# Optimization experiments

Measured on AMD Instinct MI355X. Metric: run time of the kernel, lower is better.

The kernel has to match this reference:

```python
import jax, jax.numpy as jnp
import numpy as np

B = 262144
HID = 256
HEADS = 8


def setup_inputs() -> dict:
    key = jax.random.key(0)
    ks = jax.random.split(key, 8)
    s = 1.0 / np.sqrt(HID)
    return {
        "fine_messages": jax.random.normal(ks[0], (B, HID), jnp.float32),
        "coarse_messages": jax.random.normal(ks[1], (B, HID), jnp.float32),
        "motif_features": jax.random.normal(ks[2], (B, HID), jnp.float32),
        "Wq": jax.random.normal(ks[3], (HID, HID), jnp.float32) * s,
        "Wk": jax.random.normal(ks[4], (HID, HID), jnp.float32) * s,
        "Wv": jax.random.normal(ks[5], (HID, HID), jnp.float32) * s,
        "Wo": jax.random.normal(ks[6], (HID, HID), jnp.float32) * s,
        "bo": jax.random.normal(ks[7], (HID,), jnp.float32) * s,
        "heads": HEADS,
    }


def reference(fine_messages, coarse_messages, motif_features, Wq, Wk, Wv, Wo, bo, heads):
    b, hid = motif_features.shape
    d_k = hid // heads
    # K/V share the same pre-projection input: [fine; coarse] -> (B, 2, hid)
    kv_in = jnp.stack([fine_messages, coarse_messages], axis=1)
    # torch Linear(x) = x @ W.T (no bias on q/k/v projections)
    q = (motif_features @ Wq.T).reshape(b, heads, d_k)          # (B, H, d_k) single query
    k = (kv_in @ Wk.T).reshape(b, 2, heads, d_k)                # (B, 2, H, d_k)
    v = (kv_in @ Wv.T).reshape(b, 2, heads, d_k)
    # NOTE: original divides by d_k, not sqrt(d_k)
    scores = jnp.einsum("bhd,bshd->bhs", q, k) / d_k            # (B, H, 2)
    att = jax.nn.softmax(scores, axis=-1)
    out = jnp.einsum("bhs,bshd->bhd", att, v).reshape(b, hid)   # (B, hid)
    return out @ Wo.T + bo
```

## Files before the change

### kernel.cpp

```cpp
#include <hip/hip_runtime.h>

#define B_TOT 262144
#define HID   256
#define NHEAD 8
#define BR    64
#define NTHR  256

typedef __bf16 bf16_t;
typedef __attribute__((ext_vector_type(8))) __bf16 bf16x8;
typedef __attribute__((ext_vector_type(4))) __bf16 bf16x4;
typedef __attribute__((ext_vector_type(4))) float  f32x4;

#define QKV_BYTES (384 * 1024)

static __device__ __forceinline__ f32x4 mfma16(bf16x8 a, bf16x8 b, f32x4 c) {
  return __builtin_amdgcn_mfma_f32_16x16x32_bf16(a, b, c, 0, 0, 0);
}

static __device__ __forceinline__ bf16x8 cvt8(float4 a, float4 b) {
  bf16x8 r;
  r[0] = (bf16_t)a.x; r[1] = (bf16_t)a.y; r[2] = (bf16_t)a.z; r[3] = (bf16_t)a.w;
  r[4] = (bf16_t)b.x; r[5] = (bf16_t)b.y; r[6] = (bf16_t)b.z; r[7] = (bf16_t)b.w;
  return r;
}

static __device__ __forceinline__ bf16x8 pin8(bf16x8 v) {
  f32x4 t = __builtin_bit_cast(f32x4, v);
  asm volatile("" : "+v"(t));
  return __builtin_bit_cast(bf16x8, t);
}

typedef __attribute__((address_space(3))) void lds_void;
typedef __attribute__((address_space(1))) void gbl_void;
static __device__ __forceinline__ void gload_lds16(const void* g, void* l) {
  __builtin_amdgcn_global_load_lds((gbl_void*)g, (lds_void*)l, 16, 0, 0);
}

__global__ __launch_bounds__(256) void pack_weights(
    const float* __restrict__ Wq, const float* __restrict__ Wk,
    const float* __restrict__ Wv, const float* __restrict__ Wo,
    bf16_t* __restrict__ ws) {
  const int t     = blockIdx.x * 256 + threadIdx.x;
  const int lane  = t & 63;
  const int chunk = t >> 6;
  const int l15 = lane & 15, lg = lane >> 4;
  const float* src;
  int row, col;
  if (chunk < 384) {
    const int slot = chunk % 6;
    const int hk   = chunk / 6;
    const int wi = slot >> 1, half = slot & 1;
    const int h = hk >> 3, ks = hk & 7;
    src = (wi == 0) ? Wq : (wi == 1) ? Wk : Wv;
    row = h * 32 + (l15 >> 2) * 8 + half * 4 + (l15 & 3);
    col = ks * 32 + lg * 8;
  } else {
    const int c  = chunk - 384;
    const int ks = c >> 4, jt = c & 15;
    src = Wo;
    row = jt * 16 + l15;
    col = ks * 32 + lg * 8;
  }
  const float* p = src + (size_t)row * HID + col;
  const float4 a = *(const float4*)p;
  const float4 b = *(const float4*)(p + 4);
  *(bf16x8*)(ws + (size_t)t * 8) = cvt8(a, b);
}

__global__ __launch_bounds__(NTHR, 2) void fused_local_aug(
    const float* __restrict__ fine, const float* __restrict__ coarse,
    const float* __restrict__ motif, const bf16_t* __restrict__ wpk,
    const float* __restrict__ bo, float* __restrict__ out) {
  __shared__ char wbuf[49152];

  const int tid  = threadIdx.x;
  const int lane = tid & 63;
  const int wave = tid >> 6;
  const int l15  = lane & 15;
  const int lg   = lane >> 4;
  const size_t row0 = (size_t)blockIdx.x * BR;
  const size_t mrow = row0 + wave * 16 + l15;

  auto stage = [&](int ph) {
    if (ph >= 24) return;
    char* dst = wbuf + (ph & 1) * 24576 + tid * 16;
    if (ph < 16) {
      const char* src = (const char*)wpk + (ph >> 1) * 49152 + (ph & 1) * 24576 + tid * 16;
#pragma unroll
      for (int i = 0; i < 6; ++i)
        gload_lds16(src + i * 4096, dst + i * 4096);
    } else {
      const char* src = (const char*)wpk + QKV_BYTES + (ph - 16) * 16384 + tid * 16;
#pragma unroll
      for (int i = 0; i < 4; ++i)
        gload_lds16(src + i * 4096, dst + i * 4096);
    }
  };

  stage(0);

  bf16x8 xm[8], xf[8], xc[8];
  {
    const float* pm = motif  + mrow * HID + lg * 8;
    const float* pf = fine   + mrow * HID + lg * 8;
    const float* pc = coarse + mrow * HID + lg * 8;
#pragma unroll
    for (int s = 0; s < 8; ++s) {
      xm[s] = pin8(cvt8(*(const float4*)(pm + s * 32), *(const float4*)(pm + s * 32 + 4)));
      xf[s] = pin8(cvt8(*(const float4*)(pf + s * 32), *(const float4*)(pf + s * 32 + 4)));
      xc[s] = pin8(cvt8(*(const float4*)(pc + s * 32), *(const float4*)(pc + s * 32 + 4)));
    }
  }
  __syncthreads();

  bf16x4 mo0[NHEAD], mo1[NHEAD];

#pragma unroll
  for (int h = 0; h < NHEAD; ++h) {
    f32x4 aQ0{}, aQ1{}, aK10{}, aK11{}, aK20{}, aK21{}, aV10{}, aV11{}, aV20{}, aV21{};
#pragma unroll
    for (int half = 0; half < 2; ++half) {
      stage(2 * h + half + 1);
      const char* pb = wbuf + ((2 * h + half) & 1) * 24576 + lane * 16;
#pragma unroll
      for (int kk = 0; kk < 4; ++kk) {
        const int ks = half * 4 + kk;
        const char* p = pb + kk * 6144;
        bf16x8 q0 = *(const bf16x8*)(p);
        bf16x8 q1 = *(const bf16x8*)(p + 1024);
        bf16x8 k0 = *(const bf16x8*)(p + 2048);
        bf16x8 k1 = *(const bf16x8*)(p + 3072);
        bf16x8 v0 = *(const bf16x8*)(p + 4096);
        bf16x8 v1 = *(const bf16x8*)(p + 5120);
        aQ0  = mfma16(q0, xm[ks], aQ0);   aQ1  = mfma16(q1, xm[ks], aQ1);
        aK10 = mfma16(k0, xf[ks], aK10);  aK11 = mfma16(k1, xf[ks], aK11);
        aK20 = mfma16(k0, xc[ks], aK20);  aK21 = mfma16(k1, xc[ks], aK21);
        aV10 = mfma16(v0, xf[ks], aV10);  aV11 = mfma16(v1, xf[ks], aV11);
        aV20 = mfma16(v0, xc[ks], aV20);  aV21 = mfma16(v1, xc[ks], aV21);
      }
      __syncthreads();
    }
    float s1 = 0.f, s2 = 0.f;
#pragma unroll
    for (int r = 0; r < 4; ++r) {
      s1 += aQ0[r] * aK10[r] + aQ1[r] * aK11[r];
      s2 += aQ0[r] * aK20[r] + aQ1[r] * aK21[r];
    }
    s1 += __shfl_xor(s1, 16); s1 += __shfl_xor(s1, 32);
    s2 += __shfl_xor(s2, 16); s2 += __shfl_xor(s2, 32);
    s1 *= (1.0f / 32.0f);  s2 *= (1.0f / 32.0f);
    const float mx = fmaxf(s1, s2);
    const float e1 = __expf(s1 - mx), e2 = __expf(s2 - mx);
    const float a1 = e1 / (e1 + e2);
    const float a2 = 1.0f - a1;
#pragma unroll
    for (int r = 0; r < 4; ++r) {
      mo0[h][r] = (bf16_t)(a1 * aV10[r] + a2 * aV20[r]);
      mo1[h][r] = (bf16_t)(a1 * aV11[r] + a2 * aV21[r]);
    }
  }

  bf16x8 mfrag[NHEAD];
#pragma unroll
  for (int h = 0; h < NHEAD; ++h) {
    bf16x8 t;
    t[0] = mo0[h][0]; t[1] = mo0[h][1]; t[2] = mo0[h][2]; t[3] = mo0[h][3];
    t[4] = mo1[h][0]; t[5] = mo1[h][1]; t[6] = mo1[h][2]; t[7] = mo1[h][3];
    mfrag[h] = t;
  }

  f32x4 acc[16];
#pragma unroll
  for (int jt = 0; jt < 16; ++jt) acc[jt] = f32x4{0.f, 0.f, 0.f, 0.f};

#pragma unroll
  for (int wp = 0; wp < 8; ++wp) {
    stage(17 + wp);
    bf16x8 mf = mfrag[wp];
    const char* pb = wbuf + (wp & 1) * 24576 + lane * 16;
#pragma unroll
    for (int jt = 0; jt < 16; ++jt) {
      bf16x8 wf = *(const bf16x8*)(pb + jt * 1024);
      acc[jt] = mfma16(wf, mf, acc[jt]);
    }
    __syncthreads();
  }

#pragma unroll
  for (int jt = 0; jt < 16; ++jt) {
    const int jj = jt * 16 + lg * 4;
    const float4 b4 = *(const float4*)(bo + jj);
    f32x4 o;
    o[0] = acc[jt][0] + b4.x;
    o[1] = acc[jt][1] + b4.y;
    o[2] = acc[jt][2] + b4.z;
    o[3] = acc[jt][3] + b4.w;
    __builtin_nontemporal_store(o, (f32x4*)(out + mrow * HID + jj));
  }
}

extern "C" void kernel_launch(void* const* d_in, const int* in_sizes, int n_in,
                              void* d_out, int out_size, void* d_ws, size_t ws_size,
                              hipStream_t stream) {
  (void)in_sizes; (void)n_in; (void)ws_size; (void)out_size;
  const float* fine   = (const float*)d_in[0];
  const float* coarse = (const float*)d_in[1];
  const float* motif  = (const float*)d_in[2];
  const float* Wq     = (const float*)d_in[3];
  const float* Wk     = (const float*)d_in[4];
  const float* Wv     = (const float*)d_in[5];
  const float* Wo     = (const float*)d_in[6];
  const float* bo     = (const float*)d_in[7];
  float* out          = (float*)d_out;
  bf16_t* wpk         = (bf16_t*)d_ws;

  pack_weights<<<128, 256, 0, stream>>>(Wq, Wk, Wv, Wo, wpk);
  fused_local_aug<<<B_TOT / BR, NTHR, 0, stream>>>(fine, coarse, motif, wpk, bo, out);
}
```

Baseline: 374.6 us.

## Make blocks persistent over eight row tiles and prefetch next tile's inputs

```diff
diff --git a/kernel.cpp b/kernel.cpp
--- a/kernel.cpp
+++ b/kernel.cpp
@@ -4,6 +4,8 @@
 #define HID   256
 #define NHEAD 8
 #define BR    64
+#define NTILE 8
+#define NBLK  512
 #define NTHR  256
 
 typedef __bf16 bf16_t;
@@ -78,11 +80,10 @@
   const int wave = tid >> 6;
   const int l15  = lane & 15;
   const int lg   = lane >> 4;
-  const size_t row0 = (size_t)blockIdx.x * BR;
-  const size_t mrow = row0 + wave * 16 + l15;
+  const size_t brow0 = (size_t)blockIdx.x * (BR * NTILE);
+  const int    wlofs = wave * 16 + l15;
 
   auto stage = [&](int ph) {
-    if (ph >= 24) return;
     char* dst = wbuf + (ph & 1) * 24576 + tid * 16;
     if (ph < 16) {
       const char* src = (const char*)wpk + (ph >> 1) * 49152 + (ph & 1) * 24576 + tid * 16;
@@ -101,6 +102,7 @@
 
   bf16x8 xm[8], xf[8], xc[8];
   {
+    const size_t mrow = brow0 + wlofs;
     const float* pm = motif  + mrow * HID + lg * 8;
     const float* pf = fine   + mrow * HID + lg * 8;
     const float* pc = coarse + mrow * HID + lg * 8;
@@ -113,89 +115,111 @@
   }
   __syncthreads();
 
-  bf16x4 mo0[NHEAD], mo1[NHEAD];
-
-#pragma unroll
-  for (int h = 0; h < NHEAD; ++h) {
-    f32x4 aQ0{}, aQ1{}, aK10{}, aK11{}, aK20{}, aK21{}, aV10{}, aV11{}, aV20{}, aV21{};
-#pragma unroll
-    for (int half = 0; half < 2; ++half) {
-      stage(2 * h + half + 1);
-      const char* pb = wbuf + ((2 * h + half) & 1) * 24576 + lane * 16;
-#pragma unroll
-      for (int kk = 0; kk < 4; ++kk) {
-        const int ks = half * 4 + kk;
-        const char* p = pb + kk * 6144;
-        bf16x8 q0 = *(const bf16x8*)(p);
-        bf16x8 q1 = *(const bf16x8*)(p + 1024);
-        bf16x8 k0 = *(const bf16x8*)(p + 2048);
-        bf16x8 k1 = *(const bf16x8*)(p + 3072);
-        bf16x8 v0 = *(const bf16x8*)(p + 4096);
-        bf16x8 v1 = *(const bf16x8*)(p + 5120);
-        aQ0  = mfma16(q0, xm[ks], aQ0);   aQ1  = mfma16(q1, xm[ks], aQ1);
-        aK10 = mfma16(k0, xf[ks], aK10);  aK11 = mfma16(k1, xf[ks], aK11);
-        aK20 = mfma16(k0, xc[ks], aK20);  aK21 = mfma16(k1, xc[ks], aK21);
-        aV10 = mfma16(v0, xf[ks], aV10);  aV11 = mfma16(v1, xf[ks], aV11);
-        aV20 = mfma16(v0, xc[ks], aV20);  aV21 = mfma16(v1, xc[ks], aV21);
+#pragma unroll 1
+  for (int tile = 0; tile < NTILE; ++tile) {
+    const size_t mrow = brow0 + tile * BR + wlofs;
+
+    bf16x4 mo0[NHEAD], mo1[NHEAD];
+
+#pragma unroll
+    for (int h = 0; h < NHEAD; ++h) {
+      f32x4 aQ0{}, aQ1{}, aK10{}, aK11{}, aK20{}, aK21{}, aV10{}, aV11{}, aV20{}, aV21{};
+#pragma unroll
+      for (int half = 0; half < 2; ++half) {
+        stage(2 * h + half + 1);
+        const char* pb = wbuf + ((2 * h + half) & 1) * 24576 + lane * 16;
+#pragma unroll
+        for (int kk = 0; kk < 4; ++kk) {
+          const int ks = half * 4 + kk;
+          const char* p = pb + kk * 6144;
+          bf16x8 q0 = *(const bf16x8*)(p);
+          bf16x8 q1 = *(const bf16x8*)(p + 1024);
+          bf16x8 k0 = *(const bf16x8*)(p + 2048);
+          bf16x8 k1 = *(const bf16x8*)(p + 3072);
+          bf16x8 v0 = *(const bf16x8*)(p + 4096);
+          bf16x8 v1 = *(const bf16x8*)(p + 5120);
+          aQ0  = mfma16(q0, xm[ks], aQ0);   aQ1  = mfma16(q1, xm[ks], aQ1);
+          aK10 = mfma16(k0, xf[ks], aK10);  aK11 = mfma16(k1, xf[ks], aK11);
+          aK20 = mfma16(k0, xc[ks], aK20);  aK21 = mfma16(k1, xc[ks], aK21);
+          aV10 = mfma16(v0, xf[ks], aV10);  aV11 = mfma16(v1, xf[ks], aV11);
+          aV20 = mfma16(v0, xc[ks], aV20);  aV21 = mfma16(v1, xc[ks], aV21);
+        }
+        __syncthreads();
+      }
+      float s1 = 0.f, s2 = 0.f;
+#pragma unroll
+      for (int r = 0; r < 4; ++r) {
+        s1 += aQ0[r] * aK10[r] + aQ1[r] * aK11[r];
+        s2 += aQ0[r] * aK20[r] + aQ1[r] * aK21[r];
+      }
+      s1 += __shfl_xor(s1, 16); s1 += __shfl_xor(s1, 32);
+      s2 += __shfl_xor(s2, 16); s2 += __shfl_xor(s2, 32);
+      s1 *= (1.0f / 32.0f);  s2 *= (1.0f / 32.0f);
+      const float mx = fmaxf(s1, s2);
+      const float e1 = __expf(s1 - mx), e2 = __expf(s2 - mx);
+      const float a1 = e1 / (e1 + e2);
+      const float a2 = 1.0f - a1;
+#pragma unroll
+      for (int r = 0; r < 4; ++r) {
+        mo0[h][r] = (bf16_t)(a1 * aV10[r] + a2 * aV20[r]);
+        mo1[h][r] = (bf16_t)(a1 * aV11[r] + a2 * aV21[r]);
+      }
+    }
+
+    bf16x8 mfrag[NHEAD];
+#pragma unroll
+    for (int h = 0; h < NHEAD; ++h) {
+      bf16x8 t;
+      t[0] = mo0[h][0]; t[1] = mo0[h][1]; t[2] = mo0[h][2]; t[3] = mo0[h][3];
+      t[4] = mo1[h][0]; t[5] = mo1[h][1]; t[6] = mo1[h][2]; t[7] = mo1[h][3];
+      mfrag[h] = t;
+    }
+
+    f32x4 acc[16];
+#pragma unroll
+    for (int jt = 0; jt < 16; ++jt) acc[jt] = f32x4{0.f, 0.f, 0.f, 0.f};
+
+    const bool more = (tile + 1 < NTILE);
+    const size_t nrow = mrow + BR;
+    const float* npm = motif  + nrow * HID + lg * 8;
+    const float* npf = fine   + nrow * HID + lg * 8;
+    const float* npc = coarse + nrow * HID + lg * 8;
+
+#pragma unroll
+    for (int wp = 0; wp < 8; ++wp) {
+      float4 nm0, nm1, nf0, nf1, nc0, nc1;
+      if (more) {
+        nm0 = *(const float4*)(npm + wp * 32); nm1 = *(const float4*)(npm + wp * 32 + 4);
+        nf0 = *(const float4*)(npf + wp * 32); nf1 = *(const float4*)(npf + wp * 32 + 4);
+        nc0 = *(const float4*)(npc + wp * 32); nc1 = *(const float4*)(npc + wp * 32 + 4);
+      }
+      stage((17 + wp) % 24);
+      bf16x8 mf = mfrag[wp];
+      const char* pb = wbuf + (wp & 1) * 24576 + lane * 16;
+#pragma unroll
+      for (int jt = 0; jt < 16; ++jt) {
+        bf16x8 wf = *(const bf16x8*)(pb + jt * 1024);
+        acc[jt] = mfma16(wf, mf, acc[jt]);
+      }
+      if (more) {
+        xm[wp] = pin8(cvt8(nm0, nm1));
+        xf[wp] = pin8(cvt8(nf0, nf1));
+        xc[wp] = pin8(cvt8(nc0, nc1));
       }
       __syncthreads();
     }
-    float s1 = 0.f, s2 = 0.f;
-#pragma unroll
-    for (int r = 0; r < 4; ++r) {
-      s1 += aQ0[r] * aK10[r] + aQ1[r] * aK11[r];
-      s2 += aQ0[r] * aK20[r] + aQ1[r] * aK21[r];
-    }
-    s1 += __shfl_xor(s1, 16); s1 += __shfl_xor(s1, 32);
-    s2 += __shfl_xor(s2, 16); s2 += __shfl_xor(s2, 32);
-    s1 *= (1.0f / 32.0f);  s2 *= (1.0f / 32.0f);
-    const float mx = fmaxf(s1, s2);
-    const float e1 = __expf(s1 - mx), e2 = __expf(s2 - mx);
-    const float a1 = e1 / (e1 + e2);
-    const float a2 = 1.0f - a1;
-#pragma unroll
-    for (int r = 0; r < 4; ++r) {
-      mo0[h][r] = (bf16_t)(a1 * aV10[r] + a2 * aV20[r]);
-      mo1[h][r] = (bf16_t)(a1 * aV11[r] + a2 * aV21[r]);
-    }
-  }
-
-  bf16x8 mfrag[NHEAD];
-#pragma unroll
-  for (int h = 0; h < NHEAD; ++h) {
-    bf16x8 t;
-    t[0] = mo0[h][0]; t[1] = mo0[h][1]; t[2] = mo0[h][2]; t[3] = mo0[h][3];
-    t[4] = mo1[h][0]; t[5] = mo1[h][1]; t[6] = mo1[h][2]; t[7] = mo1[h][3];
-    mfrag[h] = t;
-  }
-
-  f32x4 acc[16];
-#pragma unroll
-  for (int jt = 0; jt < 16; ++jt) acc[jt] = f32x4{0.f, 0.f, 0.f, 0.f};
-
-#pragma unroll
-  for (int wp = 0; wp < 8; ++wp) {
-    stage(17 + wp);
-    bf16x8 mf = mfrag[wp];
-    const char* pb = wbuf + (wp & 1) * 24576 + lane * 16;
+
 #pragma unroll
     for (int jt = 0; jt < 16; ++jt) {
-      bf16x8 wf = *(const bf16x8*)(pb + jt * 1024);
-      acc[jt] = mfma16(wf, mf, acc[jt]);
-    }
-    __syncthreads();
-  }
-
-#pragma unroll
-  for (int jt = 0; jt < 16; ++jt) {
-    const int jj = jt * 16 + lg * 4;
-    const float4 b4 = *(const float4*)(bo + jj);
-    f32x4 o;
-    o[0] = acc[jt][0] + b4.x;
-    o[1] = acc[jt][1] + b4.y;
-    o[2] = acc[jt][2] + b4.z;
-    o[3] = acc[jt][3] + b4.w;
-    __builtin_nontemporal_store(o, (f32x4*)(out + mrow * HID + jj));
+      const int jj = jt * 16 + lg * 4;
+      const float4 b4 = *(const float4*)(bo + jj);
+      f32x4 o;
+      o[0] = acc[jt][0] + b4.x;
+      o[1] = acc[jt][1] + b4.y;
+      o[2] = acc[jt][2] + b4.z;
+      o[3] = acc[jt][3] + b4.w;
+      __builtin_nontemporal_store(o, (f32x4*)(out + mrow * HID + jj));
+    }
   }
 }
 
@@ -215,5 +239,5 @@
   bf16_t* wpk         = (bf16_t*)d_ws;
 
   pack_weights<<<128, 256, 0, stream>>>(Wq, Wk, Wv, Wo, wpk);
-  fused_local_aug<<<B_TOT / BR, NTHR, 0, stream>>>(fine, coarse, motif, wpk, bo, out);
-}
+  fused_local_aug<<<NBLK, NTHR, 0, stream>>>(fine, coarse, motif, wpk, bo, out);
+}
```

Result: slower. 1.088 ms (+190.4%).

## Triple-buffer weight staging with explicit vmcnt waits and single barrier per phase

Applied to the files above, without the earlier changes.

```diff
diff --git a/kernel.cpp b/kernel.cpp
--- a/kernel.cpp
+++ b/kernel.cpp
@@ -12,6 +12,13 @@
 typedef __attribute__((ext_vector_type(4))) float  f32x4;
 
 #define QKV_BYTES (384 * 1024)
+
+#define PHASE_SYNC(N)                                                  \
+  do {                                                                 \
+    asm volatile("s_waitcnt vmcnt(" #N ") lgkmcnt(0)" ::: "memory");   \
+    __builtin_amdgcn_s_barrier();                                      \
+    __builtin_amdgcn_sched_barrier(0);                                 \
+  } while (0)
 
 static __device__ __forceinline__ f32x4 mfma16(bf16x8 a, bf16x8 b, f32x4 c) {
   return __builtin_amdgcn_mfma_f32_16x16x32_bf16(a, b, c, 0, 0, 0);
@@ -71,7 +78,7 @@
     const float* __restrict__ fine, const float* __restrict__ coarse,
     const float* __restrict__ motif, const bf16_t* __restrict__ wpk,
     const float* __restrict__ bo, float* __restrict__ out) {
-  __shared__ char wbuf[49152];
+  __shared__ char wbuf[73728];
 
   const int tid  = threadIdx.x;
   const int lane = tid & 63;
@@ -82,8 +89,7 @@
   const size_t mrow = row0 + wave * 16 + l15;
 
   auto stage = [&](int ph) {
-    if (ph >= 24) return;
-    char* dst = wbuf + (ph & 1) * 24576 + tid * 16;
+    char* dst = wbuf + (ph % 3) * 24576 + tid * 16;
     if (ph < 16) {
       const char* src = (const char*)wpk + (ph >> 1) * 49152 + (ph & 1) * 24576 + tid * 16;
 #pragma unroll
@@ -98,6 +104,7 @@
   };
 
   stage(0);
+  stage(1);
 
   bf16x8 xm[8], xf[8], xc[8];
   {
@@ -120,25 +127,29 @@
     f32x4 aQ0{}, aQ1{}, aK10{}, aK11{}, aK20{}, aK21{}, aV10{}, aV11{}, aV20{}, aV21{};
 #pragma unroll
     for (int half = 0; half < 2; ++half) {
-      stage(2 * h + half + 1);
-      const char* pb = wbuf + ((2 * h + half) & 1) * 24576 + lane * 16;
+      const int p = 2 * h + half;
+      if (p > 0) {
+        if (p == 15) { PHASE_SYNC(4); }
+        else         { PHASE_SYNC(6); }
+      }
+      stage(p + 2);
+      const char* pb = wbuf + (p % 3) * 24576 + lane * 16;
 #pragma unroll
       for (int kk = 0; kk < 4; ++kk) {
         const int ks = half * 4 + kk;
-        const char* p = pb + kk * 6144;
-        bf16x8 q0 = *(const bf16x8*)(p);
-        bf16x8 q1 = *(const bf16x8*)(p + 1024);
-        bf16x8 k0 = *(const bf16x8*)(p + 2048);
-        bf16x8 k1 = *(const bf16x8*)(p + 3072);
-        bf16x8 v0 = *(const bf16x8*)(p + 4096);
-        bf16x8 v1 = *(const bf16x8*)(p + 5120);
+        const char* q = pb + kk * 6144;
+        bf16x8 q0 = *(const bf16x8*)(q);
+        bf16x8 q1 = *(const bf16x8*)(q + 1024);
+        bf16x8 k0 = *(const bf16x8*)(q + 2048);
+        bf16x8 k1 = *(const bf16x8*)(q + 3072);
+        bf16x8 v0 = *(const bf16x8*)(q + 4096);
+        bf16x8 v1 = *(const bf16x8*)(q + 5120);
         aQ0  = mfma16(q0, xm[ks], aQ0);   aQ1  = mfma16(q1, xm[ks], aQ1);
         aK10 = mfma16(k0, xf[ks], aK10);  aK11 = mfma16(k1, xf[ks], aK11);
         aK20 = mfma16(k0, xc[ks], aK20);  aK21 = mfma16(k1, xc[ks], aK21);
         aV10 = mfma16(v0, xf[ks], aV10);  aV11 = mfma16(v1, xf[ks], aV11);
         aV20 = mfma16(v0, xc[ks], aV20);  aV21 = mfma16(v1, xc[ks], aV21);
       }
-      __syncthreads();
     }
     float s1 = 0.f, s2 = 0.f;
 #pragma unroll
@@ -175,15 +186,17 @@
 
 #pragma unroll
   for (int wp = 0; wp < 8; ++wp) {
-    stage(17 + wp);
+    const int p = 16 + wp;
+    if (wp == 7) { PHASE_SYNC(0); }
+    else         { PHASE_SYNC(4); }
+    if (wp < 6) stage(p + 2);
     bf16x8 mf = mfrag[wp];
-    const char* pb = wbuf + (wp & 1) * 24576 + lane * 16;
+    const char* pb = wbuf + (p % 3) * 24576 + lane * 16;
 #pragma unroll
     for (int jt = 0; jt < 16; ++jt) {
       bf16x8 wf = *(const bf16x8*)(pb + jt * 1024);
       acc[jt] = mfma16(wf, mf, acc[jt]);
     }
-    __syncthreads();
   }
 
 #pragma unroll
```

New measurement: 357.1 us. -4.7%, faster.
